# Optimization experiments

Measured on AMD Instinct MI355X. Metric: run time of the kernel, lower is better.

## Reference

```python
import jax, jax.numpy as jnp
import numpy as np

TABLE_SIZE = 256
N_EMBD = 768
B, T = 2, 1024
VOCAB = TABLE_SIZE * TABLE_SIZE


def setup_inputs() -> dict:
    key = jax.random.key(0)
    k1, k2, k3, k4 = jax.random.split(key, 4)
    hidden_states = jax.random.normal(k1, (B, T, N_EMBD), dtype=jnp.float32)
    target_ids = jax.random.randint(k2, (B, T), 0, VOCAB, dtype=jnp.int32).astype(jnp.int64)
    W_row = jax.random.normal(k3, (TABLE_SIZE, N_EMBD), dtype=jnp.float32) * 0.02
    b_row = jnp.zeros((TABLE_SIZE,), dtype=jnp.float32)
    col_weight = jax.random.normal(k4, (TABLE_SIZE, N_EMBD, TABLE_SIZE), dtype=jnp.float32) * 0.02
    col_bias = jnp.zeros((TABLE_SIZE, TABLE_SIZE), dtype=jnp.float32)
    return {
        "hidden_states": hidden_states,
        "target_ids": target_ids,
        "W_row": W_row,
        "b_row": b_row,
        "col_weight": col_weight,
        "col_bias": col_bias,
    }


def reference(hidden_states, target_ids, W_row, b_row, col_weight, col_bias):
    table_size = col_weight.shape[0]
    # row head: (B,T,R)
    row_logits = jnp.einsum("btd,rd->btr", hidden_states, W_row) + b_row
    # codebook.lookup: factor token id over table_size x table_size grid
    row_ids = (target_ids // table_size).reshape(-1)  # (N,)
    col_ids = (target_ids % table_size).reshape(-1)   # (N,)
    hs_flat = hidden_states.reshape(-1, hidden_states.shape[-1])  # (N,d)
    # per-token hard-routed column projection (the gather + baddbmm)
    W_tok = col_weight[row_ids]                       # (N,d,C)
    col_logits = jnp.einsum("nd,ndc->nc", hs_flat, W_tok) + col_bias[row_ids]
    # cross-entropy losses (mean over tokens)
    lp_row = jax.nn.log_softmax(row_logits.reshape(-1, table_size), axis=-1)
    loss_row = -jnp.take_along_axis(lp_row, row_ids[:, None], axis=1).mean()
    lp_col = jax.nn.log_softmax(col_logits, axis=-1)
    loss_col = -jnp.take_along_axis(lp_col, col_ids[:, None], axis=1).mean()
    return loss_row + loss_col
```

## Files before the change

kernel.cpp:

```cpp
#include <hip/hip_runtime.h>
#include <math.h>

#define TABLE 256
#define DIM   768
#define NCH   6
#define DCH   128
#define KTOK  12
#define CAP   64

__device__ __forceinline__ float2 f2zero() { return make_float2(0.f, 0.f); }

__global__ __launch_bounds__(256) void k_ztrans(
    const float* __restrict__ Wrow,
    float* __restrict__ WrowT,
    int* __restrict__ counts)
{
    const int d = blockIdx.x;
    const int c = threadIdx.x;
    if (d == 0) counts[c] = 0;
    WrowT[(size_t)d * TABLE + c] = Wrow[(size_t)c * DIM + d];
}

__global__ __launch_bounds__(256) void k_bucket(
    const int* __restrict__ tgt, int ntok,
    int* __restrict__ counts, int* __restrict__ bucket)
{
    const int n = blockIdx.x * 256 + threadIdx.x;
    if (n >= ntok) return;
    const int r = tgt[n] >> 8;
    const int pos = atomicAdd(&counts[r], 1);
    if (pos < CAP) bucket[r * CAP + pos] = n;
}

__device__ __forceinline__ void stream_pass(
    const float* __restrict__ slab,
    const float* __restrict__ hs,
    const int* tk,
    int nvalid,
    int dbase,
    int cbase,
    float4 (*hs_lds)[DCH / 4],
    float* __restrict__ outp,
    int lane)
{
    const int half = lane >> 5;
    const int q    = lane & 31;
    __syncthreads();
    #pragma unroll
    for (int i = 0; i < KTOK / 2; ++i) {
        const int tt = (half == 0) ? tk[2 * i] : tk[2 * i + 1];
        const float4 v = *reinterpret_cast<const float4*>(
            hs + (size_t)tt * DIM + dbase + 4 * q);
        hs_lds[2 * i + half][q] = v;
    }
    __syncthreads();

    float2 acc[KTOK];
    #pragma unroll
    for (int j = 0; j < KTOK; ++j) acc[j] = f2zero();

    const float* sl = slab + cbase + 2 * lane;

    #pragma unroll 2
    for (int dq = 0; dq < DCH / 4; ++dq) {
        float4 hv[KTOK];
        #pragma unroll
        for (int j = 0; j < KTOK; ++j) hv[j] = hs_lds[j][dq];
        #pragma unroll
        for (int dd = 0; dd < 4; ++dd) {
            const float2 wv = *reinterpret_cast<const float2*>(
                sl + (size_t)(dq * 4 + dd) * TABLE);
            #pragma unroll
            for (int j = 0; j < KTOK; ++j) {
                const float h = (dd == 0) ? hv[j].x : (dd == 1) ? hv[j].y
                              : (dd == 2) ? hv[j].z : hv[j].w;
                acc[j].x = fmaf(h, wv.x, acc[j].x);
                acc[j].y = fmaf(h, wv.y, acc[j].y);
            }
        }
    }

    #pragma unroll
    for (int j = 0; j < KTOK; ++j)
        if (j < nvalid)
            *reinterpret_cast<float2*>(outp + (size_t)tk[j] * TABLE + cbase + 2 * lane)
                = acc[j];
}

__global__ __launch_bounds__(64) void k_stream(
    const float* __restrict__ hs,
    const float* __restrict__ WrowT,
    const float* __restrict__ CW,
    const int* __restrict__ counts,
    const int* __restrict__ bucket,
    float* __restrict__ row_part,
    float* __restrict__ col_part,
    int ntok)
{
    __shared__ float4 hs_lds[KTOK][DCH / 4];

    const int bid  = blockIdx.x;
    const int lane = threadIdx.x;
    const int ncol = 256 * NCH * 2;
    int tk[KTOK];

    if (bid < ncol) {
        const int r     = bid & 255;
        const int rest  = bid >> 8;
        const int chunk = rest >> 1;
        const int cbase = (rest & 1) * 128;
        const int cnt = min(counts[r], CAP);
        if (cnt == 0) return;
        const float* slab = CW + (size_t)r * DIM * TABLE + (size_t)chunk * DCH * TABLE;
        float* outp = col_part + (size_t)chunk * ntok * TABLE;
        for (int base = 0; base < cnt; base += KTOK) {
            #pragma unroll
            for (int j = 0; j < KTOK; ++j) {
                const int idx = (base + j < cnt) ? (base + j) : base;
                tk[j] = __builtin_amdgcn_readfirstlane(bucket[r * CAP + idx]);
            }
            stream_pass(slab, hs, tk, min(KTOK, cnt - base),
                        chunk * DCH, cbase, hs_lds, outp, lane);
        }
    } else {
        const int b      = bid - ncol;
        const int ntiles = (ntok + KTOK - 1) / KTOK;
        if (b >= ntiles * NCH * 2) return;
        const int tile   = b % ntiles;
        const int rest   = b / ntiles;
        const int chunk  = rest >> 1;
        const int cbase  = (rest & 1) * 128;
        const int cnt    = min(KTOK, ntok - tile * KTOK);
        #pragma unroll
        for (int j = 0; j < KTOK; ++j) {
            const int idx = (j < cnt) ? j : 0;
            tk[j] = tile * KTOK + idx;
        }
        const float* slab = WrowT + (size_t)chunk * DCH * TABLE;
        float* outp = row_part + (size_t)chunk * ntok * TABLE;
        stream_pass(slab, hs, tk, cnt, chunk * DCH, cbase, hs_lds, outp, lane);
    }
}

__device__ __forceinline__ float wave_nll(float4 v, int target, int lane) {
    float m = fmaxf(fmaxf(v.x, v.y), fmaxf(v.z, v.w));
    #pragma unroll
    for (int off = 32; off > 0; off >>= 1) m = fmaxf(m, __shfl_xor(m, off));
    float e = expf(v.x - m) + expf(v.y - m) + expf(v.z - m) + expf(v.w - m);
    float lt = 0.f;
    if (lane == (target >> 2)) {
        const int j = target & 3;
        lt = (j == 0) ? v.x : (j == 1) ? v.y : (j == 2) ? v.z : v.w;
    }
    #pragma unroll
    for (int off = 32; off > 0; off >>= 1) {
        e  += __shfl_xor(e, off);
        lt += __shfl_xor(lt, off);
    }
    return m + logf(e) - lt;
}

__global__ __launch_bounds__(256) void k_nll2(
    const float* __restrict__ row_part,
    const float* __restrict__ col_part,
    const float* __restrict__ brow,
    const float* __restrict__ cbias,
    const int* __restrict__ tgt, int ntok,
    float* __restrict__ per_tok)
{
    const int n = blockIdx.x * 4 + (threadIdx.x >> 6);
    if (n >= ntok) return;
    const int lane = threadIdx.x & 63;
    const int t = tgt[n];
    const int r = t >> 8;

    float4 rl = reinterpret_cast<const float4*>(brow)[lane];
    float4 cl = reinterpret_cast<const float4*>(cbias + (size_t)r * TABLE)[lane];
    #pragma unroll
    for (int ch = 0; ch < NCH; ++ch) {
        const float4 a = reinterpret_cast<const float4*>(
            row_part + ((size_t)ch * ntok + n) * TABLE)[lane];
        const float4 b = reinterpret_cast<const float4*>(
            col_part + ((size_t)ch * ntok + n) * TABLE)[lane];
        rl.x += a.x; rl.y += a.y; rl.z += a.z; rl.w += a.w;
        cl.x += b.x; cl.y += b.y; cl.z += b.z; cl.w += b.w;
    }
    const float lr = wave_nll(rl, r, lane);
    const float lc = wave_nll(cl, t & 255, lane);
    if (lane == 0) per_tok[n] = lr + lc;
}

__global__ __launch_bounds__(256) void k_reduce(
    const float* __restrict__ per_tok, int ntok, float* __restrict__ out)
{
    __shared__ float red[256];
    const int c = threadIdx.x;
    float s = 0.f;
    for (int i = c; i < ntok; i += 256) s += per_tok[i];
    red[c] = s;
    __syncthreads();
    #pragma unroll
    for (int k = 128; k > 0; k >>= 1) {
        if (c < k) red[c] += red[c + k];
        __syncthreads();
    }
    if (c == 0) out[0] = red[0] / (float)ntok;
}

extern "C" void kernel_launch(void* const* d_in, const int* in_sizes, int n_in,
                              void* d_out, int out_size, void* d_ws, size_t ws_size,
                              hipStream_t stream) {
    const float* hs    = (const float*)d_in[0];
    const int*   tgt   = (const int*)d_in[1];
    const float* Wrow  = (const float*)d_in[2];
    const float* brow  = (const float*)d_in[3];
    const float* CW    = (const float*)d_in[4];
    const float* cbias = (const float*)d_in[5];
    float* out = (float*)d_out;

    const int ntok = in_sizes[1];

    char* ws = (char*)d_ws;
    int*   counts   = (int*)(ws);
    int*   bucket   = (int*)(ws + 1024);
    float* WrowT    = (float*)(ws + 1024 + 256 * CAP * 4);
    char*  p0       = (char*)WrowT + (size_t)DIM * TABLE * 4;
    float* row_part = (float*)p0;
    float* col_part = row_part + (size_t)NCH * ntok * TABLE;
    float* per_tok  = col_part + (size_t)NCH * ntok * TABLE;

    const int ntiles = (ntok + KTOK - 1) / KTOK;
    const int nblk   = 256 * NCH * 2 + ntiles * NCH * 2;

    k_ztrans <<<DIM, 256, 0, stream>>>(Wrow, WrowT, counts);
    k_bucket <<<(ntok + 255) / 256, 256, 0, stream>>>(tgt, ntok, counts, bucket);
    k_stream <<<nblk, 64, 0, stream>>>(hs, WrowT, CW, counts, bucket,
                                       row_part, col_part, ntok);
    k_nll2   <<<(ntok + 3) / 4, 256, 0, stream>>>(row_part, col_part, brow, cbias,
                                                  tgt, ntok, per_tok);
    k_reduce <<<1, 256, 0, stream>>>(per_tok, ntok, out);
}
```

Measured before the change: 71.82 us.

## Merge prep kernels and accumulate partial logits with atomics

Folds the transpose, bucketing (now done per row with wave ballots instead of global atomics) and bias initialisation into one prep kernel. The stream kernel atomically adds its per-chunk partial logits into a single logits buffer, replacing the six-way partial buffers. The NLL kernel then reads one buffer and atomically accumulates the scaled loss, which removes the separate reduce kernel. This cuts two launches and the partial-buffer traffic, at the cost of many float atomics and a nondeterministic summation order.

Result: slower. 117.0 us (+62.9%).

```diff
diff --git a/kernel.cpp b/kernel.cpp
--- a/kernel.cpp
+++ b/kernel.cpp
@@ -10,26 +10,50 @@
 
 __device__ __forceinline__ float2 f2zero() { return make_float2(0.f, 0.f); }
 
-__global__ __launch_bounds__(256) void k_ztrans(
+__global__ __launch_bounds__(256) void k_prep(
     const float* __restrict__ Wrow,
+    const int*   __restrict__ tgt,
+    const float* __restrict__ brow,
+    const float* __restrict__ cbias,
     float* __restrict__ WrowT,
-    int* __restrict__ counts)
-{
-    const int d = blockIdx.x;
-    const int c = threadIdx.x;
-    if (d == 0) counts[c] = 0;
-    WrowT[(size_t)d * TABLE + c] = Wrow[(size_t)c * DIM + d];
-}
-
-__global__ __launch_bounds__(256) void k_bucket(
-    const int* __restrict__ tgt, int ntok,
-    int* __restrict__ counts, int* __restrict__ bucket)
-{
-    const int n = blockIdx.x * 256 + threadIdx.x;
-    if (n >= ntok) return;
-    const int r = tgt[n] >> 8;
-    const int pos = atomicAdd(&counts[r], 1);
-    if (pos < CAP) bucket[r * CAP + pos] = n;
+    int*   __restrict__ counts,
+    int*   __restrict__ bucket,
+    float* __restrict__ row_logits,
+    float* __restrict__ col_logits,
+    float* __restrict__ out, int ntok)
+{
+    const int bid = blockIdx.x;
+    const int tid = threadIdx.x;
+
+    if (bid < DIM) {
+        WrowT[(size_t)bid * TABLE + tid] = Wrow[(size_t)tid * DIM + bid];
+    } else if (bid == DIM) {
+        if (tid == 0) out[0] = 0.f;
+    } else if (bid < DIM + 1 + TABLE) {
+        if (tid >= 64) return;
+        const int r    = bid - DIM - 1;
+        const int lane = tid;
+        int pos = 0;
+        for (int c0 = 0; c0 < ntok; c0 += 64) {
+            const int n   = c0 + lane;
+            const int rid = (n < ntok) ? (tgt[n] >> 8) : -1;
+            const unsigned long long mask = __ballot(rid == r);
+            const int myoff = __popcll(mask & ((1ull << lane) - 1ull));
+            if (rid == r && pos + myoff < CAP) bucket[r * CAP + pos + myoff] = n;
+            pos += (int)__popcll(mask);
+        }
+        if (lane == 0) counts[r] = min(pos, CAP);
+    } else {
+        const int idx = bid - (DIM + 1 + TABLE);
+        const int n   = idx * 4 + (tid >> 6);
+        if (n >= ntok) return;
+        const int lane = tid & 63;
+        const int r = tgt[n] >> 8;
+        reinterpret_cast<float4*>(row_logits + (size_t)n * TABLE)[lane] =
+            reinterpret_cast<const float4*>(brow)[lane];
+        reinterpret_cast<float4*>(col_logits + (size_t)n * TABLE)[lane] =
+            reinterpret_cast<const float4*>(cbias + (size_t)r * TABLE)[lane];
+    }
 }
 
 __device__ __forceinline__ void stream_pass(
@@ -39,7 +63,7 @@
     int nvalid,
     int dbase,
     int cbase,
-    float4 (*hs_lds)[DCH / 4],
+    float* hs_lds,
     float* __restrict__ outp,
     int lane)
 {
@@ -51,7 +75,7 @@
         const int tt = (half == 0) ? tk[2 * i] : tk[2 * i + 1];
         const float4 v = *reinterpret_cast<const float4*>(
             hs + (size_t)tt * DIM + dbase + 4 * q);
-        hs_lds[2 * i + half][q] = v;
+        *reinterpret_cast<float4*>(hs_lds + (2 * i + half) * DCH + 4 * q) = v;
     }
     __syncthreads();
 
@@ -65,7 +89,8 @@
     for (int dq = 0; dq < DCH / 4; ++dq) {
         float4 hv[KTOK];
         #pragma unroll
-        for (int j = 0; j < KTOK; ++j) hv[j] = hs_lds[j][dq];
+        for (int j = 0; j < KTOK; ++j)
+            hv[j] = *reinterpret_cast<const float4*>(hs_lds + j * DCH + 4 * dq);
         #pragma unroll
         for (int dd = 0; dd < 4; ++dd) {
             const float2 wv = *reinterpret_cast<const float2*>(
@@ -82,9 +107,11 @@
 
     #pragma unroll
     for (int j = 0; j < KTOK; ++j)
-        if (j < nvalid)
-            *reinterpret_cast<float2*>(outp + (size_t)tk[j] * TABLE + cbase + 2 * lane)
-                = acc[j];
+        if (j < nvalid) {
+            float* dst = outp + (size_t)tk[j] * TABLE + cbase + 2 * lane;
+            atomicAdd(dst,     acc[j].x);
+            atomicAdd(dst + 1, acc[j].y);
+        }
 }
 
 __global__ __launch_bounds__(64) void k_stream(
@@ -93,11 +120,11 @@
     const float* __restrict__ CW,
     const int* __restrict__ counts,
     const int* __restrict__ bucket,
-    float* __restrict__ row_part,
-    float* __restrict__ col_part,
+    float* __restrict__ row_logits,
+    float* __restrict__ col_logits,
     int ntok)
 {
-    __shared__ float4 hs_lds[KTOK][DCH / 4];
+    __shared__ float hs_lds[KTOK * DCH];
 
     const int bid  = blockIdx.x;
     const int lane = threadIdx.x;
@@ -112,7 +139,6 @@
         const int cnt = min(counts[r], CAP);
         if (cnt == 0) return;
         const float* slab = CW + (size_t)r * DIM * TABLE + (size_t)chunk * DCH * TABLE;
-        float* outp = col_part + (size_t)chunk * ntok * TABLE;
         for (int base = 0; base < cnt; base += KTOK) {
             #pragma unroll
             for (int j = 0; j < KTOK; ++j) {
@@ -120,7 +146,7 @@
                 tk[j] = __builtin_amdgcn_readfirstlane(bucket[r * CAP + idx]);
             }
             stream_pass(slab, hs, tk, min(KTOK, cnt - base),
-                        chunk * DCH, cbase, hs_lds, outp, lane);
+                        chunk * DCH, cbase, hs_lds, col_logits, lane);
         }
     } else {
         const int b      = bid - ncol;
@@ -137,8 +163,7 @@
             tk[j] = tile * KTOK + idx;
         }
         const float* slab = WrowT + (size_t)chunk * DCH * TABLE;
-        float* outp = row_part + (size_t)chunk * ntok * TABLE;
-        stream_pass(slab, hs, tk, cnt, chunk * DCH, cbase, hs_lds, outp, lane);
+        stream_pass(slab, hs, tk, cnt, chunk * DCH, cbase, hs_lds, row_logits, lane);
     }
 }
 
@@ -160,51 +185,22 @@
     return m + logf(e) - lt;
 }
 
-__global__ __launch_bounds__(256) void k_nll2(
-    const float* __restrict__ row_part,
-    const float* __restrict__ col_part,
-    const float* __restrict__ brow,
-    const float* __restrict__ cbias,
-    const int* __restrict__ tgt, int ntok,
-    float* __restrict__ per_tok)
+__global__ __launch_bounds__(256) void k_nll(
+    const float* __restrict__ row_logits,
+    const float* __restrict__ col_logits,
+    const int* __restrict__ tgt, int ntok, float inv_ntok,
+    float* __restrict__ out)
 {
     const int n = blockIdx.x * 4 + (threadIdx.x >> 6);
     if (n >= ntok) return;
     const int lane = threadIdx.x & 63;
     const int t = tgt[n];
-    const int r = t >> 8;
-
-    float4 rl = reinterpret_cast<const float4*>(brow)[lane];
-    float4 cl = reinterpret_cast<const float4*>(cbias + (size_t)r * TABLE)[lane];
-    #pragma unroll
-    for (int ch = 0; ch < NCH; ++ch) {
-        const float4 a = reinterpret_cast<const float4*>(
-            row_part + ((size_t)ch * ntok + n) * TABLE)[lane];
-        const float4 b = reinterpret_cast<const float4*>(
-            col_part + ((size_t)ch * ntok + n) * TABLE)[lane];
-        rl.x += a.x; rl.y += a.y; rl.z += a.z; rl.w += a.w;
-        cl.x += b.x; cl.y += b.y; cl.z += b.z; cl.w += b.w;
-    }
-    const float lr = wave_nll(rl, r, lane);
+
+    const float4 rl = reinterpret_cast<const float4*>(row_logits + (size_t)n * TABLE)[lane];
+    const float4 cl = reinterpret_cast<const float4*>(col_logits + (size_t)n * TABLE)[lane];
+    const float lr = wave_nll(rl, t >> 8, lane);
     const float lc = wave_nll(cl, t & 255, lane);
-    if (lane == 0) per_tok[n] = lr + lc;
-}
-
-__global__ __launch_bounds__(256) void k_reduce(
-    const float* __restrict__ per_tok, int ntok, float* __restrict__ out)
-{
-    __shared__ float red[256];
-    const int c = threadIdx.x;
-    float s = 0.f;
-    for (int i = c; i < ntok; i += 256) s += per_tok[i];
-    red[c] = s;
-    __syncthreads();
-    #pragma unroll
-    for (int k = 128; k > 0; k >>= 1) {
-        if (c < k) red[c] += red[c + k];
-        __syncthreads();
-    }
-    if (c == 0) out[0] = red[0] / (float)ntok;
+    if (lane == 0) atomicAdd(out, (lr + lc) * inv_ntok);
 }
 
 extern "C" void kernel_launch(void* const* d_in, const int* in_sizes, int n_in,
@@ -221,22 +217,21 @@
     const int ntok = in_sizes[1];
 
     char* ws = (char*)d_ws;
-    int*   counts   = (int*)(ws);
-    int*   bucket   = (int*)(ws + 1024);
-    float* WrowT    = (float*)(ws + 1024 + 256 * CAP * 4);
-    char*  p0       = (char*)WrowT + (size_t)DIM * TABLE * 4;
-    float* row_part = (float*)p0;
-    float* col_part = row_part + (size_t)NCH * ntok * TABLE;
-    float* per_tok  = col_part + (size_t)NCH * ntok * TABLE;
-
-    const int ntiles = (ntok + KTOK - 1) / KTOK;
-    const int nblk   = 256 * NCH * 2 + ntiles * NCH * 2;
-
-    k_ztrans <<<DIM, 256, 0, stream>>>(Wrow, WrowT, counts);
-    k_bucket <<<(ntok + 255) / 256, 256, 0, stream>>>(tgt, ntok, counts, bucket);
-    k_stream <<<nblk, 64, 0, stream>>>(hs, WrowT, CW, counts, bucket,
-                                       row_part, col_part, ntok);
-    k_nll2   <<<(ntok + 3) / 4, 256, 0, stream>>>(row_part, col_part, brow, cbias,
-                                                  tgt, ntok, per_tok);
-    k_reduce <<<1, 256, 0, stream>>>(per_tok, ntok, out);
-}
+    int*   counts     = (int*)(ws);
+    int*   bucket     = (int*)(ws + 1024);
+    float* WrowT      = (float*)(ws + 1024 + 256 * CAP * 4);
+    char*  p0         = (char*)WrowT + (size_t)DIM * TABLE * 4;
+    float* row_logits = (float*)p0;
+    float* col_logits = row_logits + (size_t)ntok * TABLE;
+
+    const int ntiles  = (ntok + KTOK - 1) / KTOK;
+    const int nblk_s  = 256 * NCH * 2 + ntiles * NCH * 2;
+    const int nblk_p  = DIM + 1 + TABLE + (ntok + 3) / 4;
+
+    k_prep  <<<nblk_p, 256, 0, stream>>>(Wrow, tgt, brow, cbias, WrowT, counts,
+                                         bucket, row_logits, col_logits, out, ntok);
+    k_stream<<<nblk_s, 64, 0, stream>>>(hs, WrowT, CW, counts, bucket,
+                                        row_logits, col_logits, ntok);
+    k_nll   <<<(ntok + 3) / 4, 256, 0, stream>>>(row_logits, col_logits, tgt,
+                                                 ntok, 1.0f / ntok, out);
+}
```
